# Kernel optimization log

Hardware: AMD Instinct MI355X
Metric: run time of the kernel (lower is better)

Reference implementation:

```python
import jax, jax.numpy as jnp
import numpy as np

D = H = W = 128  # voxel grid resolution (shape = [1,1,128,128,128] in source)
N = 2_000_000    # number of points


def splat(vals, pts, d, h, w):
    """Adjoint of trilinear F.grid_sample (align_corners=False, zeros padding).
    vals: [N] point values; pts: [N,3] normalized (x,y,z) coords in [-1,1].
    Returns [d,h,w] voxel grid with trilinear scatter-add of vals.
    """
    # unnormalize: pixel = ((coord+1)*size - 1) / 2  (align_corners=False)
    x = ((pts[:, 0] + 1.0) * w - 1.0) * 0.5
    y = ((pts[:, 1] + 1.0) * h - 1.0) * 0.5
    z = ((pts[:, 2] + 1.0) * d - 1.0) * 0.5
    x0 = jnp.floor(x); y0 = jnp.floor(y); z0 = jnp.floor(z)
    fx = x - x0; fy = y - y0; fz = z - z0
    x0i = x0.astype(jnp.int32); y0i = y0.astype(jnp.int32); z0i = z0.astype(jnp.int32)
    grid = jnp.zeros((d * h * w,), dtype=vals.dtype)
    for dz in (0, 1):
        wz = fz if dz else (1.0 - fz)
        for dy in (0, 1):
            wy = fy if dy else (1.0 - fy)
            for dx in (0, 1):
                wx = fx if dx else (1.0 - fx)
                xi = x0i + dx; yi = y0i + dy; zi = z0i + dz
                valid = (xi >= 0) & (xi < w) & (yi >= 0) & (yi < h) & (zi >= 0) & (zi < d)
                idx = jnp.where(valid, (zi * h + yi) * w + xi, 0)
                contrib = jnp.where(valid, wx * wy * wz * vals, 0.0)
                grid = grid.at[idx].add(contrib)
    return grid.reshape(d, h, w)


def huber_sum(pred, gt, delta=1.0):
    diff = pred - gt
    a = jnp.abs(diff)
    return jnp.sum(jnp.where(a <= delta, 0.5 * diff * diff, delta * (a - 0.5 * delta)))


def setup_inputs() -> dict:
    key = jax.random.key(0)
    k1, k2, k3 = jax.random.split(key, 3)
    coords = jax.random.uniform(k1, (1, N, 3), jnp.float32, -0.95, 0.95)
    registration_pred = 0.02 * jax.random.normal(k2, (1, N, 3), jnp.float32)
    registration_gt = 0.02 * jax.random.normal(k3, (1, N, 3), jnp.float32)
    return {"registration_pred": registration_pred,
            "registration_gt": registration_gt,
            "coords": coords}


def reference(registration_pred, registration_gt, coords):
    pred_pts = (coords + registration_pred).reshape(-1, 3)   # [N,3]
    gt_pts = (coords + registration_gt).reshape(-1, 3)       # [N,3]
    vals = jnp.ones((pred_pts.shape[0],), dtype=coords.dtype)
    pred_rast = splat(vals, pred_pts, D, H, W)   # [128,128,128]
    gt_rast = splat(vals, gt_pts, D, H, W)       # [128,128,128]
    return huber_sum(pred_rast, gt_rast)
```

## Files before the change

kernel.cpp:

```cpp
#include <hip/hip_runtime.h>
#include <stdint.h>

constexpr int GRID_R = 128;
constexpr int NVOX = GRID_R * GRID_R * GRID_R;

constexpr int TILE = 16;
constexpr int TPD = GRID_R / TILE;
constexpr int NBINS = TPD * TPD * TPD;
constexpr int CAP = 13312;
constexpr int CUR_STRIDE = 16;
constexpr size_t CUR_BYTES = (size_t)NBINS * CUR_STRIDE * sizeof(uint32_t);
constexpr size_t ITEMS_BYTES = (size_t)NBINS * CAP * sizeof(uint2);
constexpr size_t SORT_WS_NEEDED = CUR_BYTES + ITEMS_BYTES;

constexpr uint32_t SENT_W1 = 0xFFFFFFFFu;

constexpr int PAD = 18;

constexpr int QXB = 9;
constexpr int QZSTRIDE = QXB * QXB;
constexpr int QARR = PAD * QZSTRIDE;
constexpr float QSCALE = 1024.0f;

__device__ __forceinline__ int axis_tiles(int c0, int* ts, int* ls) {
    int n = 0;
    if ((unsigned)c0 < (unsigned)GRID_R) {
        int tx = c0 >> 4; ts[0] = tx; ls[0] = c0 - (tx << 4); n = 1;
    }
    int c1 = c0 + 1;
    if ((unsigned)c1 < (unsigned)GRID_R) {
        int tx = c1 >> 4;
        if (!n || tx != ts[0]) { ts[n] = tx; ls[n] = c0 - (tx << 4); ++n; }
    }
    return n;
}

template <typename F>
__device__ __forceinline__ void for_each_replica(float px, float py, float pz,
                                                 uint32_t g, F&& emit) {
    float x0f = floorf(px), y0f = floorf(py), z0f = floorf(pz);
    int x0 = (int)x0f, y0 = (int)y0f, z0 = (int)z0f;
    float fx = px - x0f, fy = py - y0f, fz = pz - z0f;

    int txs[2], lxs[2], tys[2], lys[2], tzs[2], lzs[2];
    int ntx = axis_tiles(x0, txs, lxs);
    int nty = axis_tiles(y0, tys, lys);
    int ntz = axis_tiles(z0, tzs, lzs);
    if (!ntx || !nty || !ntz) return;

    uint32_t ufx = (uint32_t)(fx * 65535.0f + 0.5f);
    uint32_t ufy = (uint32_t)(fy * 65535.0f + 0.5f);
    uint32_t ufz = (uint32_t)(fz * 65535.0f + 0.5f);
    uint32_t w0 = ufx | (ufy << 16);

    for (int c = 0; c < ntz; ++c)
        for (int b = 0; b < nty; ++b)
            for (int a = 0; a < ntx; ++a) {
                int bin = (tzs[c] * TPD + tys[b]) * TPD + txs[a];
                uint32_t w1 = ufz |
                              ((uint32_t)(lxs[a] + 1) << 16) |
                              ((uint32_t)(lys[b] + 1) << 21) |
                              ((uint32_t)(lzs[c] + 1) << 26) |
                              (g << 31);
                emit(bin, w0, w1);
            }
}

__device__ __forceinline__ void load_pts(const float* __restrict__ pred_reg,
                                         const float* __restrict__ gt_reg,
                                         const float* __restrict__ coords,
                                         int i, float* pa, float* pb) {
    float cx = coords[3 * i + 0], cy = coords[3 * i + 1], cz = coords[3 * i + 2];
    pa[0] = (cx + pred_reg[3 * i + 0] + 1.0f) * 64.0f - 0.5f;
    pa[1] = (cy + pred_reg[3 * i + 1] + 1.0f) * 64.0f - 0.5f;
    pa[2] = (cz + pred_reg[3 * i + 2] + 1.0f) * 64.0f - 0.5f;
    pb[0] = (cx + gt_reg[3 * i + 0] + 1.0f) * 64.0f - 0.5f;
    pb[1] = (cy + gt_reg[3 * i + 1] + 1.0f) * 64.0f - 0.5f;
    pb[2] = (cz + gt_reg[3 * i + 2] + 1.0f) * 64.0f - 0.5f;
}

#define SBLOCK 1024
#define PPT 4
constexpr int RCAP = 16;

__global__ __launch_bounds__(SBLOCK) void scatter_kernel(
        const float* __restrict__ pred_reg, const float* __restrict__ gt_reg,
        const float* __restrict__ coords, uint32_t* __restrict__ cursors,
        uint2* __restrict__ items, float* __restrict__ out, int n) {
    __shared__ alignas(16) uint2 ring[NBINS * RCAP];
    __shared__ uint32_t pc[NBINS];
    __shared__ uint32_t fl[NBINS];
    int t = threadIdx.x;
    if (t < NBINS) { pc[t] = 0; fl[t] = 0; }
    if (blockIdx.x == 0 && t == 0) *out = 0.0f;
    __syncthreads();

    int i0 = blockIdx.x * (SBLOCK * PPT);

    for (int k = 0; k < PPT; ++k) {
        int i = i0 + k * SBLOCK + t;
        if (i < n) {
            float pa[3], pb[3];
            load_pts(pred_reg, gt_reg, coords, i, pa, pb);
            auto emit = [&](int bin, uint32_t w0, uint32_t w1) {
                uint32_t base = fl[bin] * 8u;
                uint32_t r = atomicAdd(&pc[bin], 1u);
                if (r - base < (uint32_t)RCAP) {
                    ring[bin * RCAP + (int)(r & (RCAP - 1))] = make_uint2(w0, w1);
                } else {
                    atomicSub(&pc[bin], 1u);
                    uint32_t s = atomicAdd(&cursors[bin * CUR_STRIDE], 2u);
                    if (s + 2u <= (uint32_t)CAP) {
                        uint4* dst = (uint4*)(items + (size_t)bin * CAP + s);
                        *dst = make_uint4(w0, w1, 0u, SENT_W1);
                    }
                }
            };
            for_each_replica(pa[0], pa[1], pa[2], 0u, emit);
            for_each_replica(pb[0], pb[1], pb[2], 1u, emit);
        }
        __syncthreads();
        if (t < NBINS) {
            uint32_t f = fl[t], p = pc[t];
            uint32_t ng = (p - f * 8u) >> 3;
            if (ng) {
                uint32_t s0 = atomicAdd(&cursors[t * CUR_STRIDE], ng * 8u);
                const uint4* rsrc = (const uint4*)&ring[t * RCAP];
                for (uint32_t g = 0; g < ng; ++g) {
                    uint32_t sb = s0 + g * 8u;
                    const uint4* src = rsrc + ((int)((f + g) & 1u)) * 4;
                    if (sb + 8u <= (uint32_t)CAP) {
                        uint4* dst = (uint4*)(items + (size_t)t * CAP + sb);
                        dst[0] = src[0]; dst[1] = src[1];
                        dst[2] = src[2]; dst[3] = src[3];
                    } else {
                        int rb = t * RCAP + (int)(((f + g) & 1u) << 3);
                        for (int j = 0; j < 8; ++j)
                            if (sb + j < (uint32_t)CAP)
                                items[(size_t)t * CAP + sb + j] = ring[rb + j];
                    }
                }
                fl[t] = f + ng;
            }
        }
        __syncthreads();
    }

    if (t < NBINS) {
        uint32_t f = fl[t], p = pc[t];
        uint32_t fb = f * 8u;
        uint32_t res = p - fb;
        if (res) {
            uint32_t r2 = (res + 1u) & ~1u;
            for (uint32_t j = res; j < r2; ++j)
                ring[t * RCAP + (int)((fb + j) & (RCAP - 1))] =
                    make_uint2(0u, SENT_W1);
            uint32_t s0 = atomicAdd(&cursors[t * CUR_STRIDE], r2);
            for (uint32_t j = 0; j < r2; ++j) {
                uint32_t s = s0 + j;
                if (s < (uint32_t)CAP)
                    items[(size_t)t * CAP + s] =
                        ring[t * RCAP + (int)((fb + j) & (RCAP - 1))];
            }
        }
    }
}

#define ABLOCK 1024

__device__ __forceinline__ void accum_item(uint64_t* __restrict__ U,
                                           uint32_t wx, uint32_t wy) {
    int lx1 = (int)((wy >> 16) & 31u);
    if (lx1 == 31) return;
    float fx = (float)(wx & 0xffffu) * (1.0f / 65535.0f);
    float fy = (float)(wx >> 16) * (1.0f / 65535.0f);
    float fz = (float)(wy & 0xffffu) * (1.0f / 65535.0f);
    int ly1 = (int)((wy >> 21) & 31u);
    int lz1 = (int)((wy >> 26) & 31u);
    uint32_t g = wy >> 31;

    int px = lx1 & 1, xb = lx1 >> 1;
    int py = ly1 & 1, yb = ly1 >> 1;
    uint64_t* arr = U + ((g << 2) | (py << 1) | px) * QARR;
    int idx = lz1 * QZSTRIDE + yb * QXB + xb;

    float wx1 = fx, wx0 = 1.0f - fx;
    float wy1 = fy, wy0 = 1.0f - fy;
    float q00 = wx0 * wy0 * QSCALE, q10 = wx1 * wy0 * QSCALE;
    float q01 = wx0 * wy1 * QSCALE, q11 = wx1 * wy1 * QSCALE;
    float wz1 = fz, wz0 = 1.0f - fz;

    auto pk = [&](float wz) -> uint64_t {
        uint32_t lo = (uint32_t)(q00 * wz + 0.5f) |
                      ((uint32_t)(q10 * wz + 0.5f) << 16);
        uint32_t hi = (uint32_t)(q01 * wz + 0.5f) |
                      ((uint32_t)(q11 * wz + 0.5f) << 16);
        return (uint64_t)lo | ((uint64_t)hi << 32);
    };
    atomicAdd((unsigned long long*)&arr[idx],
              (unsigned long long)pk(wz0));
    atomicAdd((unsigned long long*)&arr[idx + QZSTRIDE],
              (unsigned long long)pk(wz1));
}

__global__ __launch_bounds__(ABLOCK, 4) void accum_kernel(
        const uint2* __restrict__ items, const uint32_t* __restrict__ cursors,
        float* __restrict__ out) {
    __shared__ uint64_t U[8 * QARR];
    __shared__ float wsum[ABLOCK / 64];
    int bin = blockIdx.x, t = threadIdx.x;

    for (int j = t; j < 8 * QARR; j += ABLOCK) U[j] = 0ull;
    __syncthreads();

    uint32_t cnt = cursors[bin * CUR_STRIDE];
    if (cnt > (uint32_t)CAP) cnt = CAP;
    const uint2* seg = items + (size_t)bin * CAP;
    const uint4* seg4 = (const uint4*)seg;
    uint32_t npair = cnt >> 1;

    uint32_t i = t;
    uint4 w = (i < npair) ? seg4[i] : make_uint4(0, 0, 0, 0);
    while (i < npair) {
        uint32_t inext = i + ABLOCK;
        uint4 wn = (inext < npair) ? seg4[inext] : make_uint4(0, 0, 0, 0);
        accum_item(U, w.x, w.y);
        accum_item(U, w.z, w.w);
        w = wn; i = inext;
    }
    if ((cnt & 1) && t == 0) {
        uint2 lw = seg[cnt - 1];
        accum_item(U, lw.x, lw.y);
    }
    __syncthreads();

    float s = 0.0f;
    for (int j = t; j < TILE * TILE * TILE; j += ABLOCK) {
        int x = (j & 15) + 1, y = ((j >> 4) & 15) + 1, z = (j >> 8) + 1;
        float v[2];
#pragma unroll
        for (int g = 0; g < 2; ++g) {
            float acc = 0.0f;
#pragma unroll
            for (int py = 0; py < 2; ++py)
#pragma unroll
                for (int px = 0; px < 2; ++px) {
                    int xb = (x - px) >> 1, lx = (x - px) & 1;
                    int yb = (y - py) >> 1, ly = (y - py) & 1;
                    uint64_t q = U[((g << 2) | (py << 1) | px) * QARR +
                                   z * QZSTRIDE + yb * QXB + xb];
                    acc += (float)((uint32_t)(q >> (((ly << 1) | lx) << 4)) &
                                   0xFFFFu);
                }
            v[g] = acc;
        }
        float d = (v[0] - v[1]) * (1.0f / QSCALE);
        float aa = fabsf(d);
        s += (aa <= 1.0f) ? 0.5f * d * d : (aa - 0.5f);
    }
#pragma unroll
    for (int off = 32; off > 0; off >>= 1) s += __shfl_down(s, off, 64);
    int lane = t & 63, wid = t >> 6;
    if (!lane) wsum[wid] = s;
    __syncthreads();
    if (!t) {
        float tot = 0.0f;
#pragma unroll
        for (int wv = 0; wv < ABLOCK / 64; ++wv) tot += wsum[wv];
        unsafeAtomicAdd(out, tot);
    }
}

__device__ __forceinline__ void splat_point(float nx, float ny, float nz,
                                            float* __restrict__ grid) {
    float x = (nx + 1.0f) * 64.0f - 0.5f;
    float y = (ny + 1.0f) * 64.0f - 0.5f;
    float z = (nz + 1.0f) * 64.0f - 0.5f;
    float x0f = floorf(x), y0f = floorf(y), z0f = floorf(z);
    float fx = x - x0f, fy = y - y0f, fz = z - z0f;
    int x0 = (int)x0f, y0 = (int)y0f, z0 = (int)z0f;
    int xs[2] = {x0, x0 + 1}, ys[2] = {y0, y0 + 1}, zs[2] = {z0, z0 + 1};
    float wxs[2] = {1.0f - fx, fx}, wys[2] = {1.0f - fy, fy}, wzs[2] = {1.0f - fz, fz};
#pragma unroll
    for (int dz = 0; dz < 2; ++dz) {
        int zi = zs[dz]; if ((unsigned)zi >= (unsigned)GRID_R) continue;
#pragma unroll
        for (int dy = 0; dy < 2; ++dy) {
            int yi = ys[dy]; if ((unsigned)yi >= (unsigned)GRID_R) continue;
            float wzy = wzs[dz] * wys[dy];
            int basei = (zi * GRID_R + yi) * GRID_R;
#pragma unroll
            for (int dx = 0; dx < 2; ++dx) {
                int xi = xs[dx]; if ((unsigned)xi >= (unsigned)GRID_R) continue;
                unsafeAtomicAdd(&grid[basei + xi], wzy * wxs[dx]);
            }
        }
    }
}

__global__ void splat_kernel(const float* __restrict__ pred_reg,
                             const float* __restrict__ gt_reg,
                             const float* __restrict__ coords,
                             float* __restrict__ gridA, float* __restrict__ gridB,
                             int n) {
    int i = blockIdx.x * blockDim.x + threadIdx.x;
    if (i >= n) return;
    float cx = coords[3 * i + 0], cy = coords[3 * i + 1], cz = coords[3 * i + 2];
    splat_point(cx + pred_reg[3 * i + 0], cy + pred_reg[3 * i + 1],
                cz + pred_reg[3 * i + 2], gridA);
    splat_point(cx + gt_reg[3 * i + 0], cy + gt_reg[3 * i + 1],
                cz + gt_reg[3 * i + 2], gridB);
}

__global__ void huber_kernel(const float4* __restrict__ A,
                             const float4* __restrict__ B,
                             float* __restrict__ out) {
    int i = blockIdx.x * blockDim.x + threadIdx.x;
    float4 a = A[i], b = B[i];
    auto h1 = [](float d) { float x = fabsf(d);
                            return (x <= 1.0f) ? 0.5f * d * d : (x - 0.5f); };
    float s = h1(a.x - b.x) + h1(a.y - b.y) + h1(a.z - b.z) + h1(a.w - b.w);
#pragma unroll
    for (int off = 32; off > 0; off >>= 1) s += __shfl_down(s, off, 64);
    __shared__ float wsum[4];
    int lane = threadIdx.x & 63, wid = threadIdx.x >> 6;
    if (!lane) wsum[wid] = s;
    __syncthreads();
    if (!threadIdx.x) atomicAdd(out, wsum[0] + wsum[1] + wsum[2] + wsum[3]);
}

extern "C" void kernel_launch(void* const* d_in, const int* in_sizes, int n_in,
                              void* d_out, int out_size, void* d_ws, size_t ws_size,
                              hipStream_t stream) {
    const float* pred_reg = (const float*)d_in[0];
    const float* gt_reg   = (const float*)d_in[1];
    const float* coords   = (const float*)d_in[2];
    float* outp = (float*)d_out;
    int n = in_sizes[2] / 3;

    if (ws_size >= SORT_WS_NEEDED) {
        uint32_t* cursors = (uint32_t*)d_ws;
        uint2* items = (uint2*)((char*)d_ws + CUR_BYTES);
        hipMemsetAsync(cursors, 0, CUR_BYTES, stream);

        int sblocks = (n + SBLOCK * PPT - 1) / (SBLOCK * PPT);
        scatter_kernel<<<sblocks, SBLOCK, 0, stream>>>(pred_reg, gt_reg, coords,
                                                       cursors, items, outp, n);
        accum_kernel<<<NBINS, ABLOCK, 0, stream>>>(items, cursors, outp);
    } else {
        hipMemsetAsync(d_out, 0, sizeof(float), stream);
        float* gridA = (float*)d_ws;
        float* gridB = gridA + NVOX;
        hipMemsetAsync(d_ws, 0, (size_t)2 * NVOX * sizeof(float), stream);
        int blocks = (n + 255) / 256;
        splat_kernel<<<blocks, 256, 0, stream>>>(pred_reg, gt_reg, coords,
                                                 gridA, gridB, n);
        huber_kernel<<<NVOX / 4 / 256, 256, 0, stream>>>((const float4*)gridA,
                                                         (const float4*)gridB, outp);
    }
}
```

Measured before the change: 159.3 us.

## Merge pred and gt accumulators into one signed biased grid

Instead of separate shared-memory accumulators for the pred and gt groups, gt contributions are negated (two's complement) and added into a single set of packed 16-bit lanes initialised with a 0x8000 bias. This halves the LDS footprint and the readback work in the Huber stage, where the net difference is read directly. Padding items now use a sentinel so they are skipped rather than adding zero. The risk is carry and borrow propagating between the packed 16-bit lanes when the net count leaves the biased range, which could corrupt neighbouring lanes.

```diff
diff --git a/kernel.cpp b/kernel.cpp
--- a/kernel.cpp
+++ b/kernel.cpp
@@ -21,6 +21,7 @@
 constexpr int QZSTRIDE = QXB * QXB;
 constexpr int QARR = PAD * QZSTRIDE;
 constexpr float QSCALE = 1024.0f;
+constexpr uint64_t QBIAS = 0x8000800080008000ull;
 
 __device__ __forceinline__ int axis_tiles(int c0, int* ts, int* ls) {
     int n = 0;
@@ -181,7 +182,7 @@
 
     int px = lx1 & 1, xb = lx1 >> 1;
     int py = ly1 & 1, yb = ly1 >> 1;
-    uint64_t* arr = U + ((g << 2) | (py << 1) | px) * QARR;
+    uint64_t* arr = U + ((py << 1) | px) * QARR;
     int idx = lz1 * QZSTRIDE + yb * QXB + xb;
 
     float wx1 = fx, wx0 = 1.0f - fx;
@@ -197,20 +198,20 @@
                       ((uint32_t)(q11 * wz + 0.5f) << 16);
         return (uint64_t)lo | ((uint64_t)hi << 32);
     };
-    atomicAdd((unsigned long long*)&arr[idx],
-              (unsigned long long)pk(wz0));
-    atomicAdd((unsigned long long*)&arr[idx + QZSTRIDE],
-              (unsigned long long)pk(wz1));
+    uint64_t p0 = pk(wz0), p1 = pk(wz1);
+    if (g) { p0 = 0ull - p0; p1 = 0ull - p1; }
+    atomicAdd((unsigned long long*)&arr[idx], (unsigned long long)p0);
+    atomicAdd((unsigned long long*)&arr[idx + QZSTRIDE], (unsigned long long)p1);
 }
 
 __global__ __launch_bounds__(ABLOCK, 4) void accum_kernel(
         const uint2* __restrict__ items, const uint32_t* __restrict__ cursors,
         float* __restrict__ out) {
-    __shared__ uint64_t U[8 * QARR];
+    __shared__ uint64_t U[4 * QARR];
     __shared__ float wsum[ABLOCK / 64];
     int bin = blockIdx.x, t = threadIdx.x;
 
-    for (int j = t; j < 8 * QARR; j += ABLOCK) U[j] = 0ull;
+    for (int j = t; j < 4 * QARR; j += ABLOCK) U[j] = QBIAS;
     __syncthreads();
 
     uint32_t cnt = cursors[bin * CUR_STRIDE];
@@ -220,10 +221,11 @@
     uint32_t npair = cnt >> 1;
 
     uint32_t i = t;
-    uint4 w = (i < npair) ? seg4[i] : make_uint4(0, 0, 0, 0);
+    uint4 w = (i < npair) ? seg4[i] : make_uint4(0, SENT_W1, 0, SENT_W1);
     while (i < npair) {
         uint32_t inext = i + ABLOCK;
-        uint4 wn = (inext < npair) ? seg4[inext] : make_uint4(0, 0, 0, 0);
+        uint4 wn = (inext < npair) ? seg4[inext]
+                                   : make_uint4(0, SENT_W1, 0, SENT_W1);
         accum_item(U, w.x, w.y);
         accum_item(U, w.z, w.w);
         w = wn; i = inext;
@@ -237,24 +239,20 @@
     float s = 0.0f;
     for (int j = t; j < TILE * TILE * TILE; j += ABLOCK) {
         int x = (j & 15) + 1, y = ((j >> 4) & 15) + 1, z = (j >> 8) + 1;
-        float v[2];
-#pragma unroll
-        for (int g = 0; g < 2; ++g) {
-            float acc = 0.0f;
-#pragma unroll
-            for (int py = 0; py < 2; ++py)
-#pragma unroll
-                for (int px = 0; px < 2; ++px) {
-                    int xb = (x - px) >> 1, lx = (x - px) & 1;
-                    int yb = (y - py) >> 1, ly = (y - py) & 1;
-                    uint64_t q = U[((g << 2) | (py << 1) | px) * QARR +
-                                   z * QZSTRIDE + yb * QXB + xb];
-                    acc += (float)((uint32_t)(q >> (((ly << 1) | lx) << 4)) &
-                                   0xFFFFu);
-                }
-            v[g] = acc;
-        }
-        float d = (v[0] - v[1]) * (1.0f / QSCALE);
+        int net = 0;
+#pragma unroll
+        for (int py = 0; py < 2; ++py)
+#pragma unroll
+            for (int px = 0; px < 2; ++px) {
+                int xb = (x - px) >> 1, lx = (x - px) & 1;
+                int yb = (y - py) >> 1, ly = (y - py) & 1;
+                uint64_t q = U[((py << 1) | px) * QARR +
+                               z * QZSTRIDE + yb * QXB + xb];
+                int v = (int)((uint32_t)(q >> (((ly << 1) | lx) << 4)) &
+                              0xFFFFu);
+                net += v - 0x8000;
+            }
+        float d = (float)net * (1.0f / QSCALE);
         float aa = fabsf(d);
         s += (aa <= 1.0f) ? 0.5f * d * d : (aa - 0.5f);
     }
```

New measurement: 157.3 us, median of 2. About the same (-1.3%).
